# Optimization experiments

Hardware: AMD Instinct MI355X
Metric: run time of the kernel (lower is better)

Reference implementation:

```python
import jax, jax.numpy as jnp
import numpy as np

V = 4096      # num codes (vocab)
D = 128       # embedding dim
K = 3         # diffusion scales
H = 4         # attn heads
FF = 128      # ff hidden
L = 2         # attn layers
NVIS = 8192   # visits
MAXC = 32     # max codes per visit
PAD = 0


def logmap0(x):
    # Poincare ball (c=1) log map at origin: artanh(||x||) * x / ||x||
    eps = 1e-7
    norm = jnp.linalg.norm(x, axis=-1, keepdims=True)
    norm_c = jnp.clip(norm, eps, 1.0 - 1e-5)
    return jnp.arctanh(norm_c) * x / jnp.maximum(norm, eps)


def layer_norm(x, g, b, eps=1e-5):
    m = jnp.mean(x, axis=-1, keepdims=True)
    v = jnp.mean((x - m) ** 2, axis=-1, keepdims=True)
    return (x - m) * jax.lax.rsqrt(v + eps) * g + b


def attn_block(x, Wqkv, bqkv, Wo, bo, W1, b1, W2, b2, g1, be1, g2, be2):
    # x: [V, D] (batch of 1, squeezed)
    hd = D // H
    qkv = x @ Wqkv.T + bqkv                      # [V, 3D]
    q, k, v = jnp.split(qkv, 3, axis=-1)
    q = q.reshape(V, H, hd)
    k = k.reshape(V, H, hd)
    v = v.reshape(V, H, hd)
    scores = jnp.einsum('shd,thd->hst', q, k) / np.sqrt(hd).astype(x.dtype)
    a = jax.nn.softmax(scores, axis=-1)          # [H, V, V]
    o = jnp.einsum('hst,thd->shd', a, v).reshape(V, D)
    attn_out = o @ Wo.T + bo
    x = layer_norm(x + attn_out, g1, be1)
    ff = jax.nn.gelu(x @ W1.T + b1) @ W2.T + b2
    return layer_norm(x + ff, g2, be2)


def setup_inputs() -> dict:
    key = jax.random.key(0)
    ks = jax.random.split(key, 20)
    inp = {}
    inp['visits'] = jax.random.randint(ks[0], (NVIS, MAXC), 0, V)
    # hyperbolic points inside unit ball
    inp['X_hyp'] = jax.random.normal(ks[1], (V, D), jnp.float32) * 0.01
    inp['kernels'] = jax.random.normal(ks[2], (K, V, V), jnp.float32) / V
    inp['proj_W'] = jax.random.normal(ks[3], (D, K * D), jnp.float32) * 0.05
    inp['proj_b'] = jnp.zeros((D,), jnp.float32)
    s = 0.05
    inp['Wqkv'] = jax.random.normal(ks[4], (L, 3 * D, D), jnp.float32) * s
    inp['bqkv'] = jnp.zeros((L, 3 * D), jnp.float32)
    inp['Wo'] = jax.random.normal(ks[5], (L, D, D), jnp.float32) * s
    inp['bo'] = jnp.zeros((L, D), jnp.float32)
    inp['W1'] = jax.random.normal(ks[6], (L, FF, D), jnp.float32) * s
    inp['b1'] = jnp.zeros((L, FF), jnp.float32)
    inp['W2'] = jax.random.normal(ks[7], (L, D, FF), jnp.float32) * s
    inp['b2'] = jnp.zeros((L, D), jnp.float32)
    inp['ln1_g'] = jnp.ones((L, D), jnp.float32)
    inp['ln1_b'] = jnp.zeros((L, D), jnp.float32)
    inp['ln2_g'] = jnp.ones((L, D), jnp.float32)
    inp['ln2_b'] = jnp.zeros((L, D), jnp.float32)
    return inp


def reference(visits, X_hyp, kernels, proj_W, proj_b, Wqkv, bqkv, Wo, bo,
              W1, b1, W2, b2, ln1_g, ln1_b, ln2_g, ln2_b):
    # ---- hyperbolic graph diffusion ----
    Z0 = logmap0(X_hyp)                              # [V, D]
    Z_scales = jnp.einsum('kuv,vd->ukd', kernels, Z0)  # [V, K, D]
    Z_cat = Z_scales.reshape(V, K * D)
    H_ = Z_cat @ proj_W.T + proj_b                   # [V, D]
    # ---- global self-attention stack ----
    for l in range(L):
        H_ = attn_block(H_, Wqkv[l], bqkv[l], Wo[l], bo[l],
                        W1[l], b1[l], W2[l], b2[l],
                        ln1_g[l], ln1_b[l], ln2_g[l], ln2_b[l])
    # ---- per-visit masked mean pooling (segment mean) ----
    mask = (visits != PAD)                           # [NVIS, MAXC]
    gathered = H_[visits] * mask[..., None]          # [NVIS, MAXC, D]
    cnt = jnp.sum(mask, axis=-1, keepdims=True).astype(H_.dtype)
    summed = jnp.sum(gathered, axis=1)               # [NVIS, D]
    return jnp.where(cnt > 0, summed / jnp.maximum(cnt, 1.0), 0.0)
```

## Files before the change

kernel.cpp:

```cpp
#include <hip/hip_runtime.h>
#include <hip/hip_bf16.h>
#include <math.h>

#define VN 4096
#define DIM 128
#define KS 3
#define NH 4
#define HD 32
#define NVIS 8192
#define MAXC 32
#define KTOT (KS*VN)
#define PITCH 136

typedef unsigned short u16;
typedef __attribute__((ext_vector_type(8))) short short8;
typedef __attribute__((ext_vector_type(4))) float f32x4;
typedef __attribute__((ext_vector_type(4))) float f4v;

__device__ __forceinline__ u16 f2b(float f){
  union { float f; unsigned u; } c; c.f = f;
  unsigned u = c.u;
  return (u16)((u + 0x7fffu + ((u >> 16) & 1u)) >> 16);
}
__device__ __forceinline__ float b2f(u16 x){
  union { float f; unsigned u; } c; c.u = ((unsigned)x) << 16; return c.f;
}
__device__ __forceinline__ unsigned cvt2(float lo, float hi){
  unsigned r;
  asm("v_cvt_pk_bf16_f32 %0, %1, %2" : "=v"(r) : "v"(lo), "v"(hi));
  return r;
}
#define MFMA16(a,b,c) __builtin_amdgcn_mfma_f32_16x16x32_bf16((a),(b),(c),0,0,0)

__global__ __launch_bounds__(256) void k_prep(const float* __restrict__ xh, u16* __restrict__ z0,
                                              const float* __restrict__ Wqkv, const float* __restrict__ Wo,
                                              const float* __restrict__ W1, const float* __restrict__ W2,
                                              u16* __restrict__ wb){
  __shared__ float xs[64][132];
  __shared__ float part[4][64];
  __shared__ float sscale[64];
  int t = threadIdx.x;
  if(blockIdx.x >= 64){
    int gt = (blockIdx.x - 64)*256 + t;
    #pragma unroll
    for(int i=0;i<2;i++){
      int e = gt + 24576*i;
      const float* s; u16* d; int ge;
      if(e < 24576){ s = Wqkv; d = wb;          ge = e; }
      else if(e < 32768){ s = Wo; d = wb + 98304;  ge = e - 24576; }
      else if(e < 40960){ s = W1; d = wb + 131072; ge = e - 32768; }
      else              { s = W2; d = wb + 163840; ge = e - 40960; }
      float4 f = *(const float4*)&s[(size_t)ge*4];
      uint2 o = { cvt2(f.x,f.y), cvt2(f.z,f.w) };
      *(uint2*)&d[(size_t)ge*4] = o;
    }
    return;
  }
  int v0 = blockIdx.x * 64;
  #pragma unroll
  for(int i=0;i<8;i++){
    int id = t + 256*i; int e = id*4; int r = e>>7; int c = e&127;
    float4 u = *(const float4*)&xh[(size_t)(v0+r)*DIM + c];
    xs[r][c+0]=u.x; xs[r][c+1]=u.y; xs[r][c+2]=u.z; xs[r][c+3]=u.w;
  }
  __syncthreads();
  int r = t & 63, q = t >> 6;
  float p = 0.f;
  #pragma unroll
  for(int c=0;c<32;c++){ float x = xs[r][q*32+c]; p += x*x; }
  part[q][r] = p;
  __syncthreads();
  if(t < 64){
    float ss = part[0][t]+part[1][t]+part[2][t]+part[3][t];
    float n = sqrtf(ss);
    float nc = fminf(fmaxf(n, 1e-7f), 1.0f - 1e-5f);
    sscale[t] = atanhf(nc) / fmaxf(n, 1e-7f);
  }
  __syncthreads();
  #pragma unroll
  for(int i=0;i<8;i++){
    int id = t + 256*i; int e = id*4; int rr = e>>7; int cc = e&127;
    float s = sscale[rr];
    uint2 o = { cvt2(xs[rr][cc+0]*s, xs[rr][cc+1]*s),
                cvt2(xs[rr][cc+2]*s, xs[rr][cc+3]*s) };
    *(uint2*)&z0[(size_t)(v0+rr)*DIM + cc] = o;
  }
}

template<bool AF32, bool BF32>
__device__ __forceinline__ void gemm_k128_t(const void* __restrict__ Agv, int lda,
                                            const void* __restrict__ Bgv, int ldb,
                                            u16 (*As)[128*72], u16 (*Bs)[128*72], f32x4 (&acc)[2][8]){
  int t = threadIdx.x;
  int w=t>>6, lane=t&63, l15=lane&15, quad=lane>>4;
  #pragma unroll
  for(int s=0;s<2;s++)
    #pragma unroll
    for(int n=0;n<8;n++) acc[s][n] = (f32x4){0.f,0.f,0.f,0.f};

  float4 af[4][2]; uint4 ai[4];
  float4 bf[4][2]; uint4 bi[4];

  auto LOAD = [&](int kb){
    #pragma unroll
    for(int i=0;i<4;i++){
      int id = t + 256*i; int row = id>>3, c8 = id&7;
      if constexpr(AF32){
        const float* Ag = (const float*)Agv;
        af[i][0] = *(const float4*)&Ag[(size_t)row*lda + kb + c8*8];
        af[i][1] = *(const float4*)&Ag[(size_t)row*lda + kb + c8*8 + 4];
      } else {
        const u16* Ag = (const u16*)Agv;
        ai[i] = *(const uint4*)&Ag[(size_t)row*lda + kb + c8*8];
      }
      if constexpr(BF32){
        const float* Bg = (const float*)Bgv;
        bf[i][0] = *(const float4*)&Bg[(size_t)row*ldb + kb + c8*8];
        bf[i][1] = *(const float4*)&Bg[(size_t)row*ldb + kb + c8*8 + 4];
      } else {
        const u16* Bg = (const u16*)Bgv;
        bi[i] = *(const uint4*)&Bg[(size_t)row*ldb + kb + c8*8];
      }
    }
  };
  auto COMMIT = [&](u16* Ad, u16* Bd){
    #pragma unroll
    for(int i=0;i<4;i++){
      int id = t + 256*i; int row = id>>3, c8 = id&7;
      if constexpr(AF32){
        uint4 p = { cvt2(af[i][0].x, af[i][0].y), cvt2(af[i][0].z, af[i][0].w),
                    cvt2(af[i][1].x, af[i][1].y), cvt2(af[i][1].z, af[i][1].w) };
        *(uint4*)&Ad[row*72 + c8*8] = p;
      } else {
        *(uint4*)&Ad[row*72 + c8*8] = ai[i];
      }
      if constexpr(BF32){
        uint4 q = { cvt2(bf[i][0].x, bf[i][0].y), cvt2(bf[i][0].z, bf[i][0].w),
                    cvt2(bf[i][1].x, bf[i][1].y), cvt2(bf[i][1].z, bf[i][1].w) };
        *(uint4*)&Bd[row*72 + c8*8] = q;
      } else {
        *(uint4*)&Bd[row*72 + c8*8] = bi[i];
      }
    }
  };
  auto COMPUTE = [&](const u16* Asb, const u16* Bsb){
    #pragma unroll
    for(int ks=0; ks<2; ks++){
      short8 a[2], b[8];
      #pragma unroll
      for(int s=0;s<2;s++) a[s] = *(const short8*)&Asb[(w*32+s*16+l15)*72 + (ks*4+quad)*8];
      #pragma unroll
      for(int n=0;n<8;n++)  b[n] = *(const short8*)&Bsb[(n*16+l15)*72 + (ks*4+quad)*8];
      #pragma unroll
      for(int s=0;s<2;s++)
        #pragma unroll
        for(int n=0;n<8;n++) acc[s][n] = MFMA16(a[s], b[n], acc[s][n]);
    }
  };

  LOAD(0);  COMMIT(As[0], Bs[0]);  __syncthreads();
  LOAD(64); COMPUTE(As[0], Bs[0]); COMMIT(As[1], Bs[1]); __syncthreads();
  COMPUTE(As[1], Bs[1]);
}

__global__ __launch_bounds__(256) void k_gproj(const float* __restrict__ projW, const u16* __restrict__ z0,
                                               u16* __restrict__ gbuf){
  __shared__ u16 As[2][128*72], Bs[2][128*72];
  int kb = blockIdx.x >> 5, vt = blockIdx.x & 31;
  f32x4 acc[2][8];
  gemm_k128_t<true,false>(projW + kb*128, 3*DIM, z0 + (size_t)vt*128*DIM, DIM, As, Bs, acc);
  int t=threadIdx.x, w=t>>6, lane=t&63, l15=lane&15, quad=lane>>4;
  #pragma unroll
  for(int s=0;s<2;s++)
    #pragma unroll
    for(int n=0;n<8;n++)
      #pragma unroll
      for(int rg=0;rg<4;rg++){
        int d = w*32 + s*16 + quad*4 + rg;
        int v = vt*128 + n*16 + l15;
        gbuf[(size_t)(d*KS + kb)*VN + v] = f2b(acc[s][n][rg]);
      }
}

__global__ __launch_bounds__(256) void k_diff(const float* __restrict__ kers, const u16* __restrict__ gbuf,
                                              u16* __restrict__ hpart){
  __shared__ u16 As[2][128*72], Bs[2][128*72];
  int t = threadIdx.x;
  int mt = blockIdx.x & 31;
  int sl = blockIdx.x >> 5;
  int w=t>>6, lane=t&63, l15=lane&15, quad=lane>>4;
  f32x4 acc[2][8];
  #pragma unroll
  for(int s=0;s<2;s++)
    #pragma unroll
    for(int n=0;n<8;n++) acc[s][n] = (f32x4){0.f,0.f,0.f,0.f};
  int k0 = sl * 768;

  f4v  fa0[4], fa1[4];
  uint4 fb[4];

  auto LOADSTEP = [&](int step){
    int kk = k0 + step*64;
    int kout = kk >> 12; int vv = kk & 4095;
    #pragma unroll
    for(int i=0;i<4;i++){
      int id = t + 256*i; int row = id>>3, c8 = id&7;
      const float* ap = &kers[((size_t)kout<<24) + (size_t)(mt*128+row)*VN + vv + c8*8];
      fa0[i] = __builtin_nontemporal_load((const f4v*)ap);
      fa1[i] = __builtin_nontemporal_load((const f4v*)(ap+4));
      fb[i]  = *(const uint4*)&gbuf[(size_t)row*KTOT + kk + c8*8];
    }
  };
  auto COMMIT = [&](u16* Ad, u16* Bd){
    #pragma unroll
    for(int i=0;i<4;i++){
      int id = t + 256*i; int row = id>>3, c8 = id&7;
      uint4 pa = { cvt2(fa0[i].x, fa0[i].y), cvt2(fa0[i].z, fa0[i].w),
                   cvt2(fa1[i].x, fa1[i].y), cvt2(fa1[i].z, fa1[i].w) };
      *(uint4*)&Ad[row*72 + c8*8] = pa;
      *(uint4*)&Bd[row*72 + c8*8] = fb[i];
    }
  };
  auto COMPUTE = [&](const u16* Asb, const u16* Bsb){
    #pragma unroll
    for(int ks=0; ks<2; ks++){
      short8 a[2], b[8];
      #pragma unroll
      for(int s=0;s<2;s++) a[s] = *(const short8*)&Asb[(w*32+s*16+l15)*72 + (ks*4+quad)*8];
      #pragma unroll
      for(int n=0;n<8;n++)  b[n] = *(const short8*)&Bsb[(n*16+l15)*72 + (ks*4+quad)*8];
      #pragma unroll
      for(int s=0;s<2;s++)
        #pragma unroll
        for(int n=0;n<8;n++) acc[s][n] = MFMA16(a[s], b[n], acc[s][n]);
    }
  };

  LOADSTEP(0);
  COMMIT(As[0], Bs[0]);
  __syncthreads();
  #pragma unroll 1
  for(int sp=0; sp<6; sp++){
    LOADSTEP(2*sp+1);
    COMPUTE(As[0], Bs[0]);
    COMMIT(As[1], Bs[1]);
    __syncthreads();
    if(sp < 5){
      LOADSTEP(2*sp+2);
      COMPUTE(As[1], Bs[1]);
      COMMIT(As[0], Bs[0]);
      __syncthreads();
    }
  }
  COMPUTE(As[1], Bs[1]);

  u16* dst = hpart + ((size_t)blockIdx.x << 14);
  #pragma unroll
  for(int s=0;s<2;s++)
    #pragma unroll
    for(int n=0;n<8;n++)
      #pragma unroll
      for(int rg=0;rg<4;rg++)
        dst[(w*32+s*16+quad*4+rg)*128 + n*16 + l15] = f2b(acc[s][n][rg]);
}

__device__ __forceinline__ void sg64_stageB(const u16* __restrict__ wb, u16* Bs){
  int t = threadIdx.x;
  #pragma unroll
  for(int i=0;i<32;i++){
    int e = t + 64*i; int row = e>>4, c16 = e&15;
    *(uint4*)&Bs[row*PITCH + c16*8] = *(const uint4*)&wb[row*128 + c16*8];
  }
}
__device__ __forceinline__ void sg64_compute(const u16* As, const u16* Bs, f32x4 (&acc)[8]){
  int lane=threadIdx.x&63, l15=lane&15, quad=lane>>4;
  #pragma unroll
  for(int n=0;n<8;n++) acc[n] = (f32x4){0.f,0.f,0.f,0.f};
  #pragma unroll
  for(int kk=0;kk<4;kk++){
    short8 a = *(const short8*)&As[l15*PITCH + kk*32 + quad*8];
    #pragma unroll
    for(int n=0;n<8;n++){
      short8 b = *(const short8*)&Bs[(n*16+l15)*PITCH + kk*32 + quad*8];
      acc[n] = MFMA16(a, b, acc[n]);
    }
  }
}
__device__ __forceinline__ void sg64_ln(f32x4 (&acc)[8], const float* __restrict__ g,
                                        const float* __restrict__ bv, int l15){
  #pragma unroll
  for(int rg=0;rg<4;rg++){
    float a=0.f, bs=0.f;
    #pragma unroll
    for(int n=0;n<8;n++){ float x = acc[n][rg]; a += x; bs += x*x; }
    #pragma unroll
    for(int off=1;off<16;off<<=1){ a += __shfl_xor(a, off, 64); bs += __shfl_xor(bs, off, 64); }
    float mean = a*(1.f/128.f);
    float var  = bs*(1.f/128.f) - mean*mean;
    float rstd = rsqrtf(var + 1e-5f);
    #pragma unroll
    for(int n=0;n<8;n++){
      int col = n*16 + l15;
      acc[n][rg] = (acc[n][rg] - mean)*rstd*g[col] + bv[col];
    }
  }
}
__device__ __forceinline__ void sg64_writeA(f32x4 (&y)[8], u16* As, int l15, int quad){
  #pragma unroll
  for(int n=0;n<8;n++)
    #pragma unroll
    for(int rg=0;rg<4;rg++)
      As[(quad*4+rg)*PITCH + n*16 + l15] = f2b(y[n][rg]);
}

__global__ __launch_bounds__(64) void k_hqkv(const u16* __restrict__ hpart, const float* __restrict__ pb,
                                             const u16* __restrict__ wq, const float* __restrict__ bq,
                                             float* __restrict__ h0, u16* __restrict__ outq){
  __shared__ u16 As[16*PITCH], Bs[128*PITCH];
  int mt = blockIdx.x;
  int t = threadIdx.x, lane=t&63, l15=lane&15, quad=lane>>4;
  #pragma unroll
  for(int i=0;i<8;i++){
    int e = t + 64*i; int row = e>>5, c4 = e&31;
    int ge = (mt*16+row)*DIM + c4*4;
    int c0 = c4*4;
    float4 r;
    r.x = pb[c0+0]; r.y = pb[c0+1]; r.z = pb[c0+2]; r.w = pb[c0+3];
    #pragma unroll
    for(int sl=0; sl<16; sl++){
      uint2 u = *(const uint2*)&hpart[((size_t)sl<<19) + ge];
      r.x += b2f((u16)(u.x & 0xffffu)); r.y += b2f((u16)(u.x >> 16));
      r.z += b2f((u16)(u.y & 0xffffu)); r.w += b2f((u16)(u.y >> 16));
    }
    *(float4*)&h0[ge] = r;
    uint2 o = { cvt2(r.x,r.y), cvt2(r.z,r.w) };
    *(uint2*)&As[row*PITCH + c0] = o;
  }
  #pragma unroll 1
  for(int nt=0; nt<3; nt++){
    sg64_stageB(wq + nt*16384, Bs);
    f32x4 acc[8]; sg64_compute(As, Bs, acc);
    #pragma unroll
    for(int n=0;n<8;n++)
      #pragma unroll
      for(int rg=0;rg<4;rg++){
        int row = mt*16 + quad*4 + rg;
        int col = nt*128 + n*16 + l15;
        outq[(size_t)row*(3*DIM) + col] = f2b(acc[n][rg] + bq[col]);
      }
  }
}

template<bool QKV>
__global__ __launch_bounds__(64) void k_layer(const float* __restrict__ opart, const float* __restrict__ mlpart,
                                              const u16* __restrict__ wo, const float* __restrict__ bo,
                                              const float* __restrict__ resf,
                                              const float* __restrict__ g1, const float* __restrict__ be1,
                                              const u16* __restrict__ w1, const float* __restrict__ b1,
                                              const u16* __restrict__ w2, const float* __restrict__ b2,
                                              const float* __restrict__ g2, const float* __restrict__ be2,
                                              float* __restrict__ outf,
                                              const u16* __restrict__ wq, const float* __restrict__ bq,
                                              u16* __restrict__ qkvout){
  __shared__ u16 As[16*PITCH], Bs[128*PITCH];
  int mt = blockIdx.x;
  int t = threadIdx.x, lane=t&63, l15=lane&15, quad=lane>>4;
  #pragma unroll
  for(int i=0;i<8;i++){
    int e = t + 64*i; int row = e>>5, c4 = e&31; int col = c4*4;
    int hh = col>>5, c0 = col&31;
    int grow = mt*16 + row;
    int hq = hh*64 + (grow>>6); int rr = grow & 63;
    const float* o0  = opart  + ((size_t)(hq*2)   << 11);
    const float* o1  = opart  + ((size_t)(hq*2+1) << 11);
    const float* ml0 = mlpart + ((size_t)(hq*2)   << 7);
    const float* ml1 = mlpart + ((size_t)(hq*2+1) << 7);
    float m0 = ml0[rr], l0 = ml0[64+rr], m1 = ml1[rr], l1 = ml1[64+rr];
    float m = fmaxf(m0, m1);
    float w0 = __expf(m0 - m), w1f = __expf(m1 - m);
    float inv = 1.f / (l0*w0 + l1*w1f);
    float4 a  = *(const float4*)&o0[rr*32 + c0];
    float4 c  = *(const float4*)&o1[rr*32 + c0];
    uint2 o = { cvt2((a.x*w0+c.x*w1f)*inv, (a.y*w0+c.y*w1f)*inv),
                cvt2((a.z*w0+c.z*w1f)*inv, (a.w*w0+c.w*w1f)*inv) };
    *(uint2*)&As[row*PITCH + col] = o;
  }
  sg64_stageB(wo, Bs);
  f32x4 acc[8]; sg64_compute(As, Bs, acc);
  #pragma unroll
  for(int n=0;n<8;n++)
    #pragma unroll
    for(int rg=0;rg<4;rg++){
      int row = mt*16 + quad*4 + rg;
      int col = n*16 + l15;
      acc[n][rg] += bo[col] + resf[(size_t)row*DIM + col];
    }
  sg64_ln(acc, g1, be1, l15);
  f32x4 y1[8];
  #pragma unroll
  for(int n=0;n<8;n++) y1[n] = acc[n];
  sg64_writeA(y1, As, l15, quad);
  sg64_stageB(w1, Bs);
  sg64_compute(As, Bs, acc);
  #pragma unroll
  for(int n=0;n<8;n++)
    #pragma unroll
    for(int rg=0;rg<4;rg++){
      int col = n*16 + l15;
      float v = acc[n][rg] + b1[col];
      float z = 0.7978845608028654f*(v + 0.044715f*v*v*v);
      float e = __expf(2.f*z);
      float th = 1.f - 2.f/(e + 1.f);
      acc[n][rg] = 0.5f*v*(1.f + th);
    }
  sg64_writeA(acc, As, l15, quad);
  sg64_stageB(w2, Bs);
  sg64_compute(As, Bs, acc);
  #pragma unroll
  for(int n=0;n<8;n++)
    #pragma unroll
    for(int rg=0;rg<4;rg++){
      int col = n*16 + l15;
      acc[n][rg] += b2[col] + y1[n][rg];
    }
  sg64_ln(acc, g2, be2, l15);
  #pragma unroll
  for(int n=0;n<8;n++)
    #pragma unroll
    for(int rg=0;rg<4;rg++){
      int row = mt*16 + quad*4 + rg;
      int col = n*16 + l15;
      outf[(size_t)row*DIM + col] = acc[n][rg];
    }
  if constexpr(QKV){
    sg64_writeA(acc, As, l15, quad);
    #pragma unroll 1
    for(int nt=0; nt<3; nt++){
      sg64_stageB(wq + nt*16384, Bs);
      f32x4 acc2[8]; sg64_compute(As, Bs, acc2);
      #pragma unroll
      for(int n=0;n<8;n++)
        #pragma unroll
        for(int rg=0;rg<4;rg++){
          int row = mt*16 + quad*4 + rg;
          int col = nt*128 + n*16 + l15;
          qkvout[(size_t)row*(3*DIM) + col] = f2b(acc2[n][rg] + bq[col]);
        }
    }
  }
}

__global__ __launch_bounds__(256) void k_attn(const u16* __restrict__ qkv, float* __restrict__ opart,
                                              float* __restrict__ mlpart){
  __shared__ u16 Qs[64*40];
  __shared__ u16 Ksh[2][128*40];
  __shared__ u16 Vt[2][32*136];
  __shared__ u16 Ps[4*16*136];
  int t=threadIdx.x;
  int b = blockIdx.x;
  int h = b>>7, qt = (b>>1)&63, half = b&1;
  int w=t>>6, lane=t&63, l15=lane&15, quad=lane>>4;
  { int r = t>>2, c = t&3;
    *(uint4*)&Qs[r*40 + c*8] = *(const uint4*)&qkv[(size_t)(qt*64+r)*(3*DIM) + h*HD + c*8];
  }
  int skey = t>>2, sc4 = t&3;
  uint4 kreg[2], vreg[2];
  #pragma unroll
  for(int i=0;i<2;i++){
    int key = skey + 64*i;
    kreg[i] = *(const uint4*)&qkv[(size_t)((size_t)(half*16)*128+key)*(3*DIM) + DIM + h*HD + sc4*8];
    vreg[i] = *(const uint4*)&qkv[(size_t)((size_t)(half*16)*128+key)*(3*DIM) + 2*DIM + h*HD + sc4*8];
  }
  #pragma unroll
  for(int i=0;i<2;i++){
    int key = skey + 64*i;
    *(uint4*)&Ksh[0][key*40 + sc4*8] = kreg[i];
    u16 tmp[8]; *(uint4*)tmp = vreg[i];
    #pragma unroll
    for(int j=0;j<8;j++) Vt[0][(sc4*8+j)*136 + key] = tmp[j];
  }
  __syncthreads();
  short8 aq = *(short8*)&Qs[(w*16+l15)*40 + quad*8];
  f32x4 oacc[2]; oacc[0]=(f32x4){0.f,0.f,0.f,0.f}; oacc[1]=(f32x4){0.f,0.f,0.f,0.f};
  float mrun[4], lrun[4];
  #pragma unroll
  for(int rg=0;rg<4;rg++){ mrun[rg] = -INFINITY; lrun[rg] = 0.f; }
  const float sc = 0.17677669529663687f;
  for(int kti=0;kti<16;kti++){
    int cur = kti&1;
    if(kti<15){
      int kt = half*16 + kti + 1;
      #pragma unroll
      for(int i=0;i<2;i++){
        int key = skey + 64*i;
        kreg[i] = *(const uint4*)&qkv[(size_t)(kt*128+key)*(3*DIM) + DIM + h*HD + sc4*8];
        vreg[i] = *(const uint4*)&qkv[(size_t)(kt*128+key)*(3*DIM) + 2*DIM + h*HD + sc4*8];
      }
    }
    f32x4 s[8];
    #pragma unroll
    for(int n=0;n<8;n++)
      s[n] = MFMA16(aq, *(short8*)&Ksh[cur][(n*16+l15)*40 + quad*8], ((f32x4){0.f,0.f,0.f,0.f}));
    float mx[4];
    #pragma unroll
    for(int rg=0;rg<4;rg++){
      float m = -INFINITY;
      #pragma unroll
      for(int n=0;n<8;n++) m = fmaxf(m, s[n][rg]);
      #pragma unroll
      for(int off=1;off<16;off<<=1) m = fmaxf(m, __shfl_xor(m, off, 64));
      mx[rg] = m;
    }
    bool grew = false;
    #pragma unroll
    for(int rg=0;rg<4;rg++) grew = grew || (mx[rg] > mrun[rg]);
    if(__any(grew)){
      #pragma unroll
      for(int rg=0;rg<4;rg++){
        float mn = fmaxf(mrun[rg], mx[rg]);
        float alpha = __expf(sc*(mrun[rg] - mn));
        mrun[rg] = mn;
        lrun[rg] *= alpha;
        oacc[0][rg] *= alpha; oacc[1][rg] *= alpha;
      }
    }
    float rs[4];
    #pragma unroll
    for(int rg=0;rg<4;rg++) rs[rg] = 0.f;
    #pragma unroll
    for(int n=0;n<8;n++)
      #pragma unroll
      for(int rg=0;rg<4;rg++){
        float p = __expf(sc*(s[n][rg] - mrun[rg]));
        s[n][rg] = p; rs[rg] += p;
      }
    #pragma unroll
    for(int rg=0;rg<4;rg++){
      #pragma unroll
      for(int off=1;off<16;off<<=1) rs[rg] += __shfl_xor(rs[rg], off, 64);
      lrun[rg] += rs[rg];
    }
    #pragma unroll
    for(int n=0;n<8;n++)
      #pragma unroll
      for(int rg=0;rg<4;rg++)
        Ps[w*16*136 + (quad*4+rg)*136 + n*16 + l15] = f2b(s[n][rg]);
    #pragma unroll
    for(int kt2=0;kt2<4;kt2++){
      short8 ap = *(short8*)&Ps[w*16*136 + l15*136 + kt2*32 + quad*8];
      #pragma unroll
      for(int n2=0;n2<2;n2++)
        oacc[n2] = MFMA16(ap, *(short8*)&Vt[cur][(n2*16+l15)*136 + kt2*32 + quad*8], oacc[n2]);
    }
    if(kti<15){
      #pragma unroll
      for(int i=0;i<2;i++){
        int key = skey + 64*i;
        *(uint4*)&Ksh[cur^1][key*40 + sc4*8] = kreg[i];
        u16 tmp[8]; *(uint4*)tmp = vreg[i];
        #pragma unroll
        for(int j=0;j<8;j++) Vt[cur^1][(sc4*8+j)*136 + key] = tmp[j];
      }
    }
    __syncthreads();
  }
  float* op = opart + ((size_t)b << 11);
  #pragma unroll
  for(int n2=0;n2<2;n2++)
    #pragma unroll
    for(int rg=0;rg<4;rg++)
      op[(w*16+quad*4+rg)*32 + n2*16 + l15] = oacc[n2][rg];
  if(l15 == 0){
    float* ml = mlpart + ((size_t)b << 7);
    #pragma unroll
    for(int rg=0;rg<4;rg++){
      int r = w*16 + quad*4 + rg;
      ml[r] = sc*mrun[rg]; ml[64 + r] = lrun[rg];
    }
  }
}

__global__ __launch_bounds__(256) void k_pool(const int* __restrict__ visits, const float* __restrict__ xf,
                                              float* __restrict__ out){
  int t = threadIdx.x;
  int vis = blockIdx.x*2 + (t>>7);
  int col = t & 127;
  float s = 0.f; int cnt = 0;
  #pragma unroll
  for(int j=0;j<MAXC;j++){
    int idx = visits[vis*MAXC + j];
    if(idx != 0){ s += xf[(size_t)idx*DIM + col]; cnt++; }
  }
  float r = (cnt > 0) ? s/(float)cnt : 0.f;
  out[(size_t)vis*DIM + col] = r;
}

extern "C" void kernel_launch(void* const* d_in, const int* in_sizes, int n_in,
                              void* d_out, int out_size, void* d_ws, size_t ws_size,
                              hipStream_t stream){
  (void)in_sizes; (void)n_in; (void)out_size; (void)ws_size;
  const int*   visits = (const int*)d_in[0];
  const float* xhyp  = (const float*)d_in[1];
  const float* kers  = (const float*)d_in[2];
  const float* projW = (const float*)d_in[3];
  const float* projb = (const float*)d_in[4];
  const float* Wqkv  = (const float*)d_in[5];
  const float* bqkv  = (const float*)d_in[6];
  const float* Wo    = (const float*)d_in[7];
  const float* bo    = (const float*)d_in[8];
  const float* W1    = (const float*)d_in[9];
  const float* b1    = (const float*)d_in[10];
  const float* W2    = (const float*)d_in[11];
  const float* b2    = (const float*)d_in[12];
  const float* g1    = (const float*)d_in[13];
  const float* be1   = (const float*)d_in[14];
  const float* g2    = (const float*)d_in[15];
  const float* be2   = (const float*)d_in[16];

  char* ws = (char*)d_ws;
  u16*   z0    = (u16*)(ws);
  u16*   gbuf  = (u16*)(ws + (1u<<20));
  float* h0    = (float*)(ws + (4u<<20));
  u16*   qkvb  = (u16*)(ws + (7u<<20));
  float* x1f   = (float*)(ws + (15u<<20));
  float* x2f   = (float*)(ws + (18u<<20));
  u16*   hpart = (u16*)(ws + (21u<<20));
  u16*   wb    = (u16*)(ws + (40u<<20));
  float* opart = (float*)(ws + (53u<<20));
  float* mlprt = (float*)(ws + (57u<<20));

  k_prep<<<160,256,0,stream>>>(xhyp, z0, Wqkv, Wo, W1, W2, wb);
  k_gproj<<<96,256,0,stream>>>(projW, z0, gbuf);
  k_diff<<<512,256,0,stream>>>(kers, gbuf, hpart);

  const u16* wq_l[2] = { wb,            wb + 49152 };
  const u16* wo_l[2] = { wb + 98304,    wb + 98304 + 16384 };
  const u16* w1_l[2] = { wb + 131072,   wb + 131072 + 16384 };
  const u16* w2_l[2] = { wb + 163840,   wb + 163840 + 16384 };

  k_hqkv<<<256,64,0,stream>>>(hpart, projb, wq_l[0], bqkv, h0, qkvb);
  k_attn<<<512,256,0,stream>>>(qkvb, opart, mlprt);
  k_layer<true><<<256,64,0,stream>>>(opart, mlprt, wo_l[0], bo, h0, g1, be1,
                                     w1_l[0], b1, w2_l[0], b2, g2, be2, x1f,
                                     wq_l[1], bqkv + 3*DIM, qkvb);
  k_attn<<<512,256,0,stream>>>(qkvb, opart, mlprt);
  k_layer<false><<<256,64,0,stream>>>(opart, mlprt, wo_l[1], bo + DIM, x1f,
                                      g1 + DIM, be1 + DIM, w1_l[1], b1 + DIM,
                                      w2_l[1], b2 + DIM, g2 + DIM, be2 + DIM, x2f,
                                      nullptr, nullptr, nullptr);
  k_pool<<<4096,256,0,stream>>>(visits, x2f, (float*)d_out);
}
```

Before: 618.1 us.

## Split split-K reduction from QKV GEMM and use two-wave row blocks

The fused hpart reduction plus QKV projection kernel is split in two. A standalone elementwise reduction kernel writes h0, and a separate QKV GEMM kernel uses 384 blocks, one per row tile and output slice, instead of 256 blocks each looping over three slices. The per-layer kernel moves from one wave per 16 rows to two waves per 32-row tile, sharing each staged weight tile across both waves, with barriers added around shared-memory reuse. This aims to cut redundant weight staging and get more parallelism in the QKV step, at the cost of an extra launch, an extra h0 round trip, fewer layer blocks (128) and added synchronisation.

```diff
diff --git a/kernel.cpp b/kernel.cpp
--- a/kernel.cpp
+++ b/kernel.cpp
@@ -264,21 +264,47 @@
         dst[(w*32+s*16+quad*4+rg)*128 + n*16 + l15] = f2b(acc[s][n][rg]);
 }
 
-__device__ __forceinline__ void sg64_stageB(const u16* __restrict__ wb, u16* Bs){
+__global__ __launch_bounds__(256) void k_hreduce(const u16* __restrict__ hpart, const float* __restrict__ pb,
+                                                 float* __restrict__ h0){
+  int idx = blockIdx.x*256 + threadIdx.x;
+  int e0 = idx*4;
+  int c0 = e0 & 127;
+  float4 r;
+  r.x = pb[c0+0]; r.y = pb[c0+1]; r.z = pb[c0+2]; r.w = pb[c0+3];
+  #pragma unroll
+  for(int sl=0; sl<16; sl++){
+    uint2 u = *(const uint2*)&hpart[((size_t)sl<<19) + e0];
+    r.x += b2f((u16)(u.x & 0xffffu)); r.y += b2f((u16)(u.x >> 16));
+    r.z += b2f((u16)(u.y & 0xffffu)); r.w += b2f((u16)(u.y >> 16));
+  }
+  *(float4*)&h0[e0] = r;
+}
+
+__device__ __forceinline__ void sg_stageB(const u16* __restrict__ wb, u16* Bs){
   int t = threadIdx.x;
   #pragma unroll
-  for(int i=0;i<32;i++){
-    int e = t + 64*i; int row = e>>4, c16 = e&15;
+  for(int i=0;i<16;i++){
+    int e = t + 128*i; int row = e>>4, c16 = e&15;
     *(uint4*)&Bs[row*PITCH + c16*8] = *(const uint4*)&wb[row*128 + c16*8];
   }
 }
-__device__ __forceinline__ void sg64_compute(const u16* As, const u16* Bs, f32x4 (&acc)[8]){
-  int lane=threadIdx.x&63, l15=lane&15, quad=lane>>4;
+__device__ __forceinline__ void sg_stageA_f(const float* __restrict__ src, int m0, u16* As){
+  int t = threadIdx.x;
+  #pragma unroll
+  for(int i=0;i<8;i++){
+    int e = t + 128*i; int row = e>>5, c4 = e&31;
+    float4 f = *(const float4*)&src[(size_t)(m0+row)*DIM + c4*4];
+    uint2 o = { cvt2(f.x,f.y), cvt2(f.z,f.w) };
+    *(uint2*)&As[row*PITCH + c4*4] = o;
+  }
+}
+__device__ __forceinline__ void sg_compute(const u16* As, const u16* Bs, f32x4 (&acc)[8]){
+  int t=threadIdx.x, w=t>>6, lane=t&63, l15=lane&15, quad=lane>>4;
   #pragma unroll
   for(int n=0;n<8;n++) acc[n] = (f32x4){0.f,0.f,0.f,0.f};
   #pragma unroll
   for(int kk=0;kk<4;kk++){
-    short8 a = *(const short8*)&As[l15*PITCH + kk*32 + quad*8];
+    short8 a = *(const short8*)&As[(w*16+l15)*PITCH + kk*32 + quad*8];
     #pragma unroll
     for(int n=0;n<8;n++){
       short8 b = *(const short8*)&Bs[(n*16+l15)*PITCH + kk*32 + quad*8];
@@ -286,8 +312,8 @@
     }
   }
 }
-__device__ __forceinline__ void sg64_ln(f32x4 (&acc)[8], const float* __restrict__ g,
-                                        const float* __restrict__ bv, int l15){
+__device__ __forceinline__ void sg_ln(f32x4 (&acc)[8], const float* __restrict__ g,
+                                      const float* __restrict__ bv, int l15){
   #pragma unroll
   for(int rg=0;rg<4;rg++){
     float a=0.f, bs=0.f;
@@ -305,71 +331,52 @@
     }
   }
 }
-__device__ __forceinline__ void sg64_writeA(f32x4 (&y)[8], u16* As, int l15, int quad){
+__device__ __forceinline__ void sg_writeA(f32x4 (&y)[8], u16* As, int w, int l15, int quad){
   #pragma unroll
   for(int n=0;n<8;n++)
     #pragma unroll
     for(int rg=0;rg<4;rg++)
-      As[(quad*4+rg)*PITCH + n*16 + l15] = f2b(y[n][rg]);
-}
-
-__global__ __launch_bounds__(64) void k_hqkv(const u16* __restrict__ hpart, const float* __restrict__ pb,
-                                             const u16* __restrict__ wq, const float* __restrict__ bq,
-                                             float* __restrict__ h0, u16* __restrict__ outq){
-  __shared__ u16 As[16*PITCH], Bs[128*PITCH];
-  int mt = blockIdx.x;
-  int t = threadIdx.x, lane=t&63, l15=lane&15, quad=lane>>4;
+      As[(w*16+quad*4+rg)*PITCH + n*16 + l15] = f2b(y[n][rg]);
+}
+
+__global__ __launch_bounds__(128) void k_qkv_s(const float* __restrict__ xb, const u16* __restrict__ wq,
+                                               const float* __restrict__ bq, u16* __restrict__ outq){
+  __shared__ u16 As[32*PITCH], Bs[128*PITCH];
+  int bx = blockIdx.x; int mt = bx & 127, nt = bx >> 7;
+  sg_stageA_f(xb, mt*32, As);
+  sg_stageB(wq + nt*16384, Bs);
+  __syncthreads();
+  f32x4 acc[8]; sg_compute(As, Bs, acc);
+  int t=threadIdx.x, w=t>>6, lane=t&63, l15=lane&15, quad=lane>>4;
+  #pragma unroll
+  for(int n=0;n<8;n++)
+    #pragma unroll
+    for(int rg=0;rg<4;rg++){
+      int row = mt*32 + w*16 + quad*4 + rg;
+      int col = nt*128 + n*16 + l15;
+      outq[(size_t)row*(3*DIM) + col] = f2b(acc[n][rg] + bq[col]);
+    }
+}
+
+template<bool QKV>
+__global__ __launch_bounds__(128) void k_layer(const float* __restrict__ opart, const float* __restrict__ mlpart,
+                                               const u16* __restrict__ wo, const float* __restrict__ bo,
+                                               const float* __restrict__ resf,
+                                               const float* __restrict__ g1, const float* __restrict__ be1,
+                                               const u16* __restrict__ w1, const float* __restrict__ b1,
+                                               const u16* __restrict__ w2, const float* __restrict__ b2,
+                                               const float* __restrict__ g2, const float* __restrict__ be2,
+                                               float* __restrict__ outf,
+                                               const u16* __restrict__ wq, const float* __restrict__ bq,
+                                               u16* __restrict__ qkvout){
+  __shared__ u16 As[32*PITCH], Bs[128*PITCH];
+  int mt = blockIdx.x; int t = threadIdx.x;
+  int w=t>>6, lane=t&63, l15=lane&15, quad=lane>>4;
   #pragma unroll
   for(int i=0;i<8;i++){
-    int e = t + 64*i; int row = e>>5, c4 = e&31;
-    int ge = (mt*16+row)*DIM + c4*4;
-    int c0 = c4*4;
-    float4 r;
-    r.x = pb[c0+0]; r.y = pb[c0+1]; r.z = pb[c0+2]; r.w = pb[c0+3];
-    #pragma unroll
-    for(int sl=0; sl<16; sl++){
-      uint2 u = *(const uint2*)&hpart[((size_t)sl<<19) + ge];
-      r.x += b2f((u16)(u.x & 0xffffu)); r.y += b2f((u16)(u.x >> 16));
-      r.z += b2f((u16)(u.y & 0xffffu)); r.w += b2f((u16)(u.y >> 16));
-    }
-    *(float4*)&h0[ge] = r;
-    uint2 o = { cvt2(r.x,r.y), cvt2(r.z,r.w) };
-    *(uint2*)&As[row*PITCH + c0] = o;
-  }
-  #pragma unroll 1
-  for(int nt=0; nt<3; nt++){
-    sg64_stageB(wq + nt*16384, Bs);
-    f32x4 acc[8]; sg64_compute(As, Bs, acc);
-    #pragma unroll
-    for(int n=0;n<8;n++)
-      #pragma unroll
-      for(int rg=0;rg<4;rg++){
-        int row = mt*16 + quad*4 + rg;
-        int col = nt*128 + n*16 + l15;
-        outq[(size_t)row*(3*DIM) + col] = f2b(acc[n][rg] + bq[col]);
-      }
-  }
-}
-
-template<bool QKV>
-__global__ __launch_bounds__(64) void k_layer(const float* __restrict__ opart, const float* __restrict__ mlpart,
-                                              const u16* __restrict__ wo, const float* __restrict__ bo,
-                                              const float* __restrict__ resf,
-                                              const float* __restrict__ g1, const float* __restrict__ be1,
-                                              const u16* __restrict__ w1, const float* __restrict__ b1,
-                                              const u16* __restrict__ w2, const float* __restrict__ b2,
-                                              const float* __restrict__ g2, const float* __restrict__ be2,
-                                              float* __restrict__ outf,
-                                              const u16* __restrict__ wq, const float* __restrict__ bq,
-                                              u16* __restrict__ qkvout){
-  __shared__ u16 As[16*PITCH], Bs[128*PITCH];
-  int mt = blockIdx.x;
-  int t = threadIdx.x, lane=t&63, l15=lane&15, quad=lane>>4;
-  #pragma unroll
-  for(int i=0;i<8;i++){
-    int e = t + 64*i; int row = e>>5, c4 = e&31; int col = c4*4;
+    int e = t + 128*i; int row = e>>5, c4 = e&31; int col = c4*4;
     int hh = col>>5, c0 = col&31;
-    int grow = mt*16 + row;
+    int grow = mt*32 + row;
     int hq = hh*64 + (grow>>6); int rr = grow & 63;
     const float* o0  = opart  + ((size_t)(hq*2)   << 11);
     const float* o1  = opart  + ((size_t)(hq*2+1) << 11);
@@ -385,23 +392,26 @@
                 cvt2((a.z*w0+c.z*w1f)*inv, (a.w*w0+c.w*w1f)*inv) };
     *(uint2*)&As[row*PITCH + col] = o;
   }
-  sg64_stageB(wo, Bs);
-  f32x4 acc[8]; sg64_compute(As, Bs, acc);
+  sg_stageB(wo, Bs);
+  __syncthreads();
+  f32x4 acc[8]; sg_compute(As, Bs, acc);
   #pragma unroll
   for(int n=0;n<8;n++)
     #pragma unroll
     for(int rg=0;rg<4;rg++){
-      int row = mt*16 + quad*4 + rg;
+      int row = mt*32 + w*16 + quad*4 + rg;
       int col = n*16 + l15;
       acc[n][rg] += bo[col] + resf[(size_t)row*DIM + col];
     }
-  sg64_ln(acc, g1, be1, l15);
+  sg_ln(acc, g1, be1, l15);
   f32x4 y1[8];
   #pragma unroll
   for(int n=0;n<8;n++) y1[n] = acc[n];
-  sg64_writeA(y1, As, l15, quad);
-  sg64_stageB(w1, Bs);
-  sg64_compute(As, Bs, acc);
+  __syncthreads();
+  sg_writeA(y1, As, w, l15, quad);
+  sg_stageB(w1, Bs);
+  __syncthreads();
+  sg_compute(As, Bs, acc);
   #pragma unroll
   for(int n=0;n<8;n++)
     #pragma unroll
@@ -413,9 +423,11 @@
       float th = 1.f - 2.f/(e + 1.f);
       acc[n][rg] = 0.5f*v*(1.f + th);
     }
-  sg64_writeA(acc, As, l15, quad);
-  sg64_stageB(w2, Bs);
-  sg64_compute(As, Bs, acc);
+  __syncthreads();
+  sg_writeA(acc, As, w, l15, quad);
+  sg_stageB(w2, Bs);
+  __syncthreads();
+  sg_compute(As, Bs, acc);
   #pragma unroll
   for(int n=0;n<8;n++)
     #pragma unroll
@@ -423,29 +435,32 @@
       int col = n*16 + l15;
       acc[n][rg] += b2[col] + y1[n][rg];
     }
-  sg64_ln(acc, g2, be2, l15);
+  sg_ln(acc, g2, be2, l15);
   #pragma unroll
   for(int n=0;n<8;n++)
     #pragma unroll
     for(int rg=0;rg<4;rg++){
-      int row = mt*16 + quad*4 + rg;
+      int row = mt*32 + w*16 + quad*4 + rg;
       int col = n*16 + l15;
       outf[(size_t)row*DIM + col] = acc[n][rg];
     }
   if constexpr(QKV){
-    sg64_writeA(acc, As, l15, quad);
+    __syncthreads();
+    sg_writeA(acc, As, w, l15, quad);
     #pragma unroll 1
     for(int nt=0; nt<3; nt++){
-      sg64_stageB(wq + nt*16384, Bs);
-      f32x4 acc2[8]; sg64_compute(As, Bs, acc2);
+      sg_stageB(wq + nt*16384, Bs);
+      __syncthreads();
+      f32x4 a2[8]; sg_compute(As, Bs, a2);
       #pragma unroll
       for(int n=0;n<8;n++)
         #pragma unroll
         for(int rg=0;rg<4;rg++){
-          int row = mt*16 + quad*4 + rg;
+          int row = mt*32 + w*16 + quad*4 + rg;
           int col = nt*128 + n*16 + l15;
-          qkvout[(size_t)row*(3*DIM) + col] = f2b(acc2[n][rg] + bq[col]);
+          qkvout[(size_t)row*(3*DIM) + col] = f2b(a2[n][rg] + bq[col]);
         }
+      __syncthreads();
     }
   }
 }
@@ -632,21 +647,22 @@
   k_prep<<<160,256,0,stream>>>(xhyp, z0, Wqkv, Wo, W1, W2, wb);
   k_gproj<<<96,256,0,stream>>>(projW, z0, gbuf);
   k_diff<<<512,256,0,stream>>>(kers, gbuf, hpart);
+  k_hreduce<<<512,256,0,stream>>>(hpart, projb, h0);
 
   const u16* wq_l[2] = { wb,            wb + 49152 };
   const u16* wo_l[2] = { wb + 98304,    wb + 98304 + 16384 };
   const u16* w1_l[2] = { wb + 131072,   wb + 131072 + 16384 };
   const u16* w2_l[2] = { wb + 163840,   wb + 163840 + 16384 };
 
-  k_hqkv<<<256,64,0,stream>>>(hpart, projb, wq_l[0], bqkv, h0, qkvb);
+  k_qkv_s<<<384,128,0,stream>>>(h0, wq_l[0], bqkv, qkvb);
   k_attn<<<512,256,0,stream>>>(qkvb, opart, mlprt);
-  k_layer<true><<<256,64,0,stream>>>(opart, mlprt, wo_l[0], bo, h0, g1, be1,
-                                     w1_l[0], b1, w2_l[0], b2, g2, be2, x1f,
-                                     wq_l[1], bqkv + 3*DIM, qkvb);
+  k_layer<true><<<128,128,0,stream>>>(opart, mlprt, wo_l[0], bo, h0, g1, be1,
+                                      w1_l[0], b1, w2_l[0], b2, g2, be2, x1f,
+                                      wq_l[1], bqkv + 3*DIM, qkvb);
   k_attn<<<512,256,0,stream>>>(qkvb, opart, mlprt);
-  k_layer<false><<<256,64,0,stream>>>(opart, mlprt, wo_l[1], bo + DIM, x1f,
-                                      g1 + DIM, be1 + DIM, w1_l[1], b1 + DIM,
-                                      w2_l[1], b2 + DIM, g2 + DIM, be2 + DIM, x2f,
-                                      nullptr, nullptr, nullptr);
+  k_layer<false><<<128,128,0,stream>>>(opart, mlprt, wo_l[1], bo + DIM, x1f,
+                                       g1 + DIM, be1 + DIM, w1_l[1], b1 + DIM,
+                                       w2_l[1], b2 + DIM, g2 + DIM, be2 + DIM, x2f,
+                                       nullptr, nullptr, nullptr);
   k_pool<<<4096,256,0,stream>>>(visits, x2f, (float*)d_out);
 }
```

Result: faster. 547.0 us (-11.5%).
